# Performance work log

Measured on AMD Instinct MI355X. Metric: run time of the kernel, lower is better.

The kernel has to match this reference:

```python
import jax, jax.numpy as jnp
import numpy as np
import math

B, N, DQ, DK, DV, H = 8, 1024, 512, 512, 512, 8


def setup_inputs() -> dict:
    key = jax.random.key(0)
    ks = jax.random.split(key, 9)
    s = 0.02
    return {
        "Q": jax.random.normal(ks[0], (B, N, DQ), jnp.float32),
        "K": jax.random.normal(ks[1], (B, N, DK), jnp.float32),
        "mask": jax.random.bernoulli(ks[2], 0.9, (B, N)).astype(jnp.float32),
        "Wq": jax.random.normal(ks[3], (DQ, DV), jnp.float32) * s,
        "bq": jnp.zeros((DV,), jnp.float32),
        "Wk": jax.random.normal(ks[4], (DK, DV), jnp.float32) * s,
        "bk": jnp.zeros((DV,), jnp.float32),
        "Wv": jax.random.normal(ks[5], (DK, DV), jnp.float32) * s,
        "bv": jnp.zeros((DV,), jnp.float32),
        "Wo": jax.random.normal(ks[6], (DV, DV), jnp.float32) * s,
        "bo": jnp.zeros((DV,), jnp.float32),
    }


def reference(Q, K, mask, Wq, bq, Wk, bk, Wv, bv, Wo, bo):
    b, n, _ = Q.shape
    dV = Wq.shape[1]
    dh = dV // H
    scale = 1.0 / math.sqrt(dV)
    m = mask[..., None]                      # [B,N,1]
    Qp = (Q @ Wq + bq) * m                   # [B,N,dV]
    Kp = (K @ Wk + bk) * m
    Vp = (K @ Wv + bv) * m
    # torch.cat(x.split(dh,2),0) == head-major stacking -> keep as [H,B,N,dh]
    q = Qp.reshape(b, n, H, dh).transpose(2, 0, 1, 3)
    k = Kp.reshape(b, n, H, dh).transpose(2, 0, 1, 3)
    v = Vp.reshape(b, n, H, dh).transpose(2, 0, 1, 3)
    S = jnp.einsum('hbnd,hbmd->hbnm', q, k) * scale   # [H,B,N,N]
    mx = jnp.max(S, axis=3, keepdims=True)            # unmasked row max (faithful)
    m1 = mask[None, :, :, None]                       # [1,B,N,1]
    m2 = mask[None, :, None, :]                       # [1,B,1,N]
    num = jnp.exp((S - mx) * m1 * m2) * m1 * m2
    A = num / (jnp.sum(num, axis=3, keepdims=True) + 1e-16)
    O = q + jnp.einsum('hbnm,hbmd->hbnd', A, v)       # residual on Q_
    O = O.transpose(1, 2, 0, 3).reshape(b, n, dV)     # un-split heads
    O = O + jax.nn.relu((O @ Wo + bo) * m)
    return O
```

## Files before the change

### kernel.cpp

```cpp
#include <hip/hip_runtime.h>

typedef short bf16x8 __attribute__((ext_vector_type(8)));
typedef float f32x4 __attribute__((ext_vector_type(4)));
typedef float f32x16 __attribute__((ext_vector_type(16)));

#define MFMA16(a, b, c) __builtin_amdgcn_mfma_f32_16x16x32_bf16((a), (b), (c), 0, 0, 0)
#define MFMA32(a, b, c) __builtin_amdgcn_mfma_f32_32x32x16_bf16((a), (b), (c), 0, 0, 0)

#define GLOAD_LDS16(g, l)                                              \
  __builtin_amdgcn_global_load_lds(                                    \
      (const __attribute__((address_space(1))) unsigned int*)(g),      \
      (__attribute__((address_space(3))) unsigned int*)(l), 16, 0, 0)

__device__ __forceinline__ unsigned short f2b(float f) {
  union { float f; unsigned int u; } x; x.f = f;
  unsigned int r = x.u + 0x7FFFu + ((x.u >> 16) & 1u);
  return (unsigned short)(r >> 16);
}
__device__ __forceinline__ float b2f(unsigned short h) {
  union { unsigned int u; float f; } x; x.u = ((unsigned int)h) << 16;
  return x.f;
}
__device__ __forceinline__ unsigned int cvtpk(float lo, float hi) {
  unsigned int r;
  asm("v_cvt_pk_bf16_f32 %0, %1, %2" : "=v"(r) : "v"(lo), "v"(hi));
  return r;
}
__device__ __forceinline__ short cvt1(float x) {
  return (short)(unsigned short)cvtpk(x, x);
}
__device__ __forceinline__ float vexp2(float x) {
  float r;
  asm("v_exp_f32 %0, %1" : "=v"(r) : "v"(x));
  return r;
}

#define SCALE2 0.06375870724f

__global__ __launch_bounds__(256) void wtrans_kernel(
    const float* __restrict__ Wq, const float* __restrict__ Wk,
    const float* __restrict__ Wv, const float* __restrict__ Wo,
    short* __restrict__ Wt) {
  __shared__ float tile[64][65];
  const int z = blockIdx.z;
  const float* W = (z == 0) ? Wq : (z == 1) ? Wk : (z == 2) ? Wv : Wo;
  const float ws = (z == 1) ? SCALE2 : 1.0f;
  const int k0 = blockIdx.x * 64, n0 = blockIdx.y * 64;
  const int t = threadIdx.x;
  const int r = t >> 4, cc = (t & 15) * 4;
#pragma unroll
  for (int it = 0; it < 4; ++it) {
    int row = r + it * 16;
    const float4 v = *(const float4*)(W + (k0 + row) * 512 + n0 + cc);
    tile[row][cc + 0] = v.x; tile[row][cc + 1] = v.y;
    tile[row][cc + 2] = v.z; tile[row][cc + 3] = v.w;
  }
  __syncthreads();
  short* out = Wt + z * (512 * 512);
#pragma unroll
  for (int it = 0; it < 4; ++it) {
    int nrow = r + it * 16;
    unsigned int u0 = cvtpk(tile[cc + 0][nrow] * ws, tile[cc + 1][nrow] * ws);
    unsigned int u1 = cvtpk(tile[cc + 2][nrow] * ws, tile[cc + 3][nrow] * ws);
    uint2 uv; uv.x = u0; uv.y = u1;
    *(uint2*)(out + (n0 + nrow) * 512 + k0 + cc) = uv;
  }
}

__global__ __launch_bounds__(256) void cvt_kernel(
    const float* __restrict__ Q, const float* __restrict__ K,
    const float* __restrict__ mask,
    short* __restrict__ Qb, short* __restrict__ Kb, short* __restrict__ mbf) {
  if (blockIdx.y == 0 && blockIdx.x < 4) {
    int i = (blockIdx.x * 256 + threadIdx.x) * 8;
    float4 a = *(const float4*)(mask + i);
    float4 bb = *(const float4*)(mask + i + 4);
    unsigned int m0 = (a.x != 0.f) ? 0x3F80u : 0u;
    unsigned int m1 = (a.y != 0.f) ? 0x3F80u : 0u;
    unsigned int m2 = (a.z != 0.f) ? 0x3F80u : 0u;
    unsigned int m3 = (a.w != 0.f) ? 0x3F80u : 0u;
    unsigned int m4 = (bb.x != 0.f) ? 0x3F80u : 0u;
    unsigned int m5 = (bb.y != 0.f) ? 0x3F80u : 0u;
    unsigned int m6 = (bb.z != 0.f) ? 0x3F80u : 0u;
    unsigned int m7 = (bb.w != 0.f) ? 0x3F80u : 0u;
    uint4 mm;
    mm.x = m0 | (m1 << 16); mm.y = m2 | (m3 << 16);
    mm.z = m4 | (m5 << 16); mm.w = m6 | (m7 << 16);
    *(uint4*)(mbf + i) = mm;
  }
  const float* src = blockIdx.y ? K : Q;
  short* dst = blockIdx.y ? Kb : Qb;
  int i = (blockIdx.x * 256 + threadIdx.x) * 8;
  float4 v0 = *(const float4*)(src + i);
  float4 v1 = *(const float4*)(src + i + 4);
  uint2 a, b;
  a.x = cvtpk(v0.x, v0.y); a.y = cvtpk(v0.z, v0.w);
  b.x = cvtpk(v1.x, v1.y); b.y = cvtpk(v1.z, v1.w);
  *(uint2*)(dst + i) = a;
  *(uint2*)(dst + i + 4) = b;
}

__device__ __forceinline__ void gemm_bf16_core(
    const short* __restrict__ A, const short* __restrict__ Wt,
    short* Lb, int m0, int t, f32x4 acc[4][4]) {
  const int lane = t & 63, w = t >> 6;
  const int c = lane & 15, g = lane >> 4;
  const int wr = w >> 1, wc = w & 1;
  const int lr = lane >> 3;
  const int sswz = ((lane & 7) ^ lr) << 3;
  const int swc = (c & 7) << 3;
  short* Al = Lb;
  short* Bl = Lb + 8192;

  for (int kt = 0; kt < 8; ++kt) {
#pragma unroll
    for (int it = 0; it < 4; ++it) {
      int row = w * 32 + it * 8;
      GLOAD_LDS16(A + (size_t)(m0 + row + lr) * 512 + kt * 64 + sswz, Al + row * 64);
      GLOAD_LDS16(Wt + (size_t)(row + lr) * 512 + kt * 64 + sswz, Bl + row * 64);
    }
    __syncthreads();
    __builtin_amdgcn_s_setprio(1);
#pragma unroll
    for (int kc = 0; kc < 2; ++kc) {
      bf16x8 af[4], bfr[4];
#pragma unroll
      for (int mi = 0; mi < 4; ++mi) {
        int r = wr * 64 + mi * 16 + c;
        af[mi] = *(const bf16x8*)(Al + r * 64 + ((kc * 32 + 8 * g) ^ swc));
      }
#pragma unroll
      for (int ni = 0; ni < 4; ++ni) {
        int r = wc * 64 + ni * 16 + c;
        bfr[ni] = *(const bf16x8*)(Bl + r * 64 + ((kc * 32 + 8 * g) ^ swc));
      }
#pragma unroll
      for (int mi = 0; mi < 4; ++mi)
#pragma unroll
        for (int ni = 0; ni < 4; ++ni)
          acc[mi][ni] = MFMA16(af[mi], bfr[ni], acc[mi][ni]);
    }
    __builtin_amdgcn_s_setprio(0);
    __syncthreads();
  }
}

__global__ __launch_bounds__(256) void proj2_kernel(
    const short* __restrict__ Qb, const short* __restrict__ Kb,
    const short* __restrict__ Wt4,
    const float* __restrict__ bq, const float* __restrict__ bk, const float* __restrict__ bv,
    const float* __restrict__ maskf,
    short* __restrict__ Qp, short* __restrict__ Kp, short* __restrict__ Vt) {
  __shared__ short Lbuf[16384];
  const int by = blockIdx.y;
  const int m0 = blockIdx.x * 128;
  const int t = threadIdx.x;
  const short* A;
  const short* Wt;
  const float* bias;
  int nbase;
  if (by < 4) { A = Qb; nbase = by * 128; Wt = Wt4 + nbase * 512; bias = bq; }
  else if (by < 8) { A = Kb; nbase = (by - 4) * 128; Wt = Wt4 + 262144 + nbase * 512; bias = bk; }
  else { A = Kb; nbase = (by - 8) * 128; Wt = Wt4 + 524288 + nbase * 512; bias = bv; }
  const float bscale = (by >= 4 && by < 8) ? SCALE2 : 1.0f;

  const f32x4 zz = {0.f, 0.f, 0.f, 0.f};
  f32x4 acc[4][4];
#pragma unroll
  for (int mi = 0; mi < 4; ++mi)
#pragma unroll
    for (int ni = 0; ni < 4; ++ni) acc[mi][ni] = zz;
  gemm_bf16_core(A, Wt, Lbuf, m0, t, acc);

  const int lane = t & 63, w = t >> 6;
  const int c = lane & 15, g = lane >> 4;
  const int wr = w >> 1, wc = w & 1;
  float mk[4][4];
#pragma unroll
  for (int mi = 0; mi < 4; ++mi) {
    int mbase = m0 + wr * 64 + mi * 16 + 4 * g;
#pragma unroll
    for (int i = 0; i < 4; ++i) mk[mi][i] = maskf[mbase + i];
  }
  float bval[4];
#pragma unroll
  for (int ni = 0; ni < 4; ++ni) bval[ni] = bias[nbase + wc * 64 + ni * 16 + c] * bscale;

  if (by < 8) {
#pragma unroll
    for (int ni = 0; ni < 4; ++ni) {
      int nloc = wc * 64 + ni * 16 + c;
#pragma unroll
      for (int mi = 0; mi < 4; ++mi) {
#pragma unroll
        for (int i = 0; i < 4; ++i) {
          int mloc = wr * 64 + mi * 16 + 4 * g + i;
          float v = (acc[mi][ni][i] + bval[ni]) * mk[mi][i];
          Lbuf[mloc * 128 + (nloc ^ ((mloc & 7) << 3))] = cvt1(v);
        }
      }
    }
    __syncthreads();
    short* outp = (by < 4) ? Qp : Kp;
    const int rrow = t >> 4, rcol = (t & 15) * 8;
#pragma unroll
    for (int p = 0; p < 8; ++p) {
      int m = p * 16 + rrow;
      bf16x8 vv = *(const bf16x8*)(Lbuf + m * 128 + (rcol ^ ((m & 7) << 3)));
      *(bf16x8*)(outp + (size_t)(m0 + m) * 512 + nbase + rcol) = vv;
    }
  } else {
#pragma unroll
    for (int ni = 0; ni < 4; ++ni) {
      int nloc = wc * 64 + ni * 16 + c;
#pragma unroll
      for (int mi = 0; mi < 4; ++mi) {
        int mloc4 = wr * 64 + mi * 16 + 4 * g;
        unsigned int lo = cvtpk((acc[mi][ni][0] + bval[ni]) * mk[mi][0],
                                (acc[mi][ni][1] + bval[ni]) * mk[mi][1]);
        unsigned int hi = cvtpk((acc[mi][ni][2] + bval[ni]) * mk[mi][2],
                                (acc[mi][ni][3] + bval[ni]) * mk[mi][3]);
        int ma = (mloc4 & 15) + (((mloc4 >> 4) ^ (nloc & 7)) << 4);
        uint2 uv; uv.x = lo; uv.y = hi;
        *(uint2*)(Lbuf + nloc * 128 + ma) = uv;
      }
    }
    __syncthreads();
    const int rrow = t >> 4, rcol = (t & 15) * 8;
#pragma unroll
    for (int p = 0; p < 8; ++p) {
      int n = p * 16 + rrow;
      int ma = (rcol & 8) + (((rcol >> 4) ^ (n & 7)) << 4);
      bf16x8 vv = *(const bf16x8*)(Lbuf + n * 128 + ma);
      int d = nbase + n;
      int hh = d >> 6, dd = d & 63;
      int mg = m0 + rcol;
      int bi = mg >> 10, seq0 = mg & 1023;
      *(bf16x8*)(Vt + ((size_t)((bi * 8 + hh) * 64 + dd)) * 1024 + seq0) = vv;
    }
  }
}

__global__ __launch_bounds__(128, 3) void attn6_kernel(
    const short* __restrict__ Qp, const short* __restrict__ Kp,
    const short* __restrict__ Vt, const float* __restrict__ mask,
    const short* __restrict__ mbf, short* __restrict__ Obb) {
  __shared__ short Kl[32 * 128];
  __shared__ short Vl[32 * 128];
  __shared__ short Ml[1024];
  const int t = threadIdx.x, lane = t & 63, w = t >> 6;
  const int q32 = lane & 31, hi = lane >> 5;
  const int hw = blockIdx.x;
  const int L = (hw & 7) * 128 + (hw >> 3);
  const int qt = L & 15, head = L >> 4;
  const int b = head & 7, h = head >> 3;
  const int n0 = qt * 64 + w * 32;

  const short* Kg = Kp + (size_t)(b * 1024) * 512 + h * 64;
  const short* Vg = Vt + (size_t)((b * 8 + h) * 64) * 1024;

  bf16x8 qf[4];
  {
    const short* qptr = Qp + ((size_t)(b * 1024 + n0 + q32) * 512 + h * 64 + 8 * hi);
#pragma unroll
    for (int kk = 0; kk < 4; ++kk) qf[kk] = *(const bf16x8*)(qptr + 16 * kk);
  }

  auto STAGE = [&](int kvt) {
    const int kr = kvt * 64;
#pragma unroll
    for (int it = 0; it < 4; ++it) {
      int rb = it * 8 + w * 4;
      int r2 = rb + (lane >> 4);
      int sx = (lane & 15) ^ (r2 & 15);
      GLOAD_LDS16(Kg + (size_t)(kr + 2 * r2 + (sx >> 3)) * 512 + (sx & 7) * 8, Kl + rb * 128);
    }
#pragma unroll
    for (int it = 0; it < 4; ++it) {
      int rb = it * 8 + w * 4;
      int rv = rb + (lane >> 4);
      int sx = (lane & 15) ^ (rv & 15);
      GLOAD_LDS16(Vg + (size_t)(2 * rv + (sx >> 3)) * 1024 + kr + (sx & 7) * 8, Vl + rb * 128);
    }
  };

  GLOAD_LDS16(mbf + b * 1024 + w * 512 + lane * 8, Ml + w * 512);
  STAGE(0);

  f32x16 o0, o1, suma;
#pragma unroll
  for (int e = 0; e < 16; ++e) { o0[e] = 0.f; o1[e] = 0.f; suma[e] = 0.f; }

#pragma unroll 1
  for (int kvt = 0; kvt < 16; ++kvt) {
    asm volatile("s_waitcnt vmcnt(0)" ::: "memory");
    __builtin_amdgcn_sched_barrier(0);
    __builtin_amdgcn_s_barrier();
    __builtin_amdgcn_sched_barrier(0);

#pragma unroll
    for (int half = 0; half < 2; ++half) {
      bf16x8 ka[4], va[2][2], mo[2];
      {
        const int kvr = 32 * half + q32;
        const int r2 = kvr >> 1;
#pragma unroll
        for (int kk = 0; kk < 4; ++kk) {
          int sx = ((((kvr & 1) << 3) | (2 * kk + hi)) ^ (r2 & 15));
          ka[kk] = *(const bf16x8*)(Kl + r2 * 128 + sx * 8);
        }
      }
#pragma unroll
      for (int ds = 0; ds < 2; ++ds) {
        const int d = 32 * ds + q32;
        const int rv = d >> 1;
#pragma unroll
        for (int ch = 0; ch < 2; ++ch) {
          int sx = ((((d & 1) << 3) | (4 * half + 2 * ch + hi)) ^ (rv & 15));
          va[ds][ch] = *(const bf16x8*)(Vl + rv * 128 + sx * 8);
        }
      }
#pragma unroll
      for (int ch = 0; ch < 2; ++ch)
        mo[ch] = *(const bf16x8*)(Ml + kvt * 64 + 32 * half + 16 * ch + 8 * hi);

      __builtin_amdgcn_sched_barrier(0);
      asm volatile("s_waitcnt lgkmcnt(0)" ::: "memory");
      __builtin_amdgcn_sched_barrier(0);
      if (half == 1) {
        __builtin_amdgcn_s_barrier();
        __builtin_amdgcn_sched_barrier(0);
        if (kvt < 15) STAGE(kvt + 1);
        __builtin_amdgcn_sched_barrier(0);
      }

      f32x16 s0;
#pragma unroll
      for (int e = 0; e < 16; ++e) s0[e] = 0.f;
      __builtin_amdgcn_s_setprio(1);
#pragma unroll
      for (int kk = 0; kk < 4; ++kk) s0 = MFMA32(ka[kk], qf[kk], s0);
      __builtin_amdgcn_s_setprio(0);

      f32x16 p0;
#pragma unroll
      for (int e = 0; e < 16; ++e) p0[e] = vexp2(s0[e]);

      bf16x8 pf[2];
#pragma unroll
      for (int ch = 0; ch < 2; ++ch) {
        unsigned int w01a = cvtpk(p0[8 * ch + 0], p0[8 * ch + 1]);
        unsigned int w01b = cvtpk(p0[8 * ch + 2], p0[8 * ch + 3]);
        unsigned int w23a = cvtpk(p0[8 * ch + 4], p0[8 * ch + 5]);
        unsigned int w23b = cvtpk(p0[8 * ch + 6], p0[8 * ch + 7]);
        unsigned int x0 = hi ? w01a : w23a;
        unsigned int x1 = hi ? w01b : w23b;
        unsigned int g0 = (unsigned int)__shfl_xor((int)x0, 32);
        unsigned int g1 = (unsigned int)__shfl_xor((int)x1, 32);
        union { unsigned int u[4]; bf16x8 v; } pu;
        pu.u[0] = hi ? g0 : w01a;
        pu.u[1] = hi ? g1 : w01b;
        pu.u[2] = hi ? w23a : g0;
        pu.u[3] = hi ? w23b : g1;
        pf[ch] = pu.v;
      }

      __builtin_amdgcn_s_setprio(1);
#pragma unroll
      for (int ch = 0; ch < 2; ++ch) {
        o0 = MFMA32(va[0][ch], pf[ch], o0);
        o1 = MFMA32(va[1][ch], pf[ch], o1);
        suma = MFMA32(mo[ch], pf[ch], suma);
      }
      __builtin_amdgcn_s_setprio(0);
    }
  }

  short* Tw = Kl + w * 2304;
  const float inv = __builtin_amdgcn_rcpf(suma[0] + 1e-16f);
#pragma unroll
  for (int rr = 0; rr < 4; ++rr) {
    uint2 uv0, uv1;
    uv0.x = cvtpk(o0[4 * rr + 0] * inv, o0[4 * rr + 1] * inv);
    uv0.y = cvtpk(o0[4 * rr + 2] * inv, o0[4 * rr + 3] * inv);
    *(uint2*)(Tw + q32 * 68 + 8 * rr + 4 * hi) = uv0;
    uv1.x = cvtpk(o1[4 * rr + 0] * inv, o1[4 * rr + 1] * inv);
    uv1.y = cvtpk(o1[4 * rr + 2] * inv, o1[4 * rr + 3] * inv);
    *(uint2*)(Tw + q32 * 68 + 32 + 8 * rr + 4 * hi) = uv1;
  }
  asm volatile("s_waitcnt lgkmcnt(0)" ::: "memory");
  __builtin_amdgcn_sched_barrier(0);

  const int erow = lane >> 1, ecs = (lane & 1) * 8;
  const float mk1 = mask[b * 1024 + n0 + erow];
#pragma unroll
  for (int it = 0; it < 4; ++it) {
    int col = ecs + it * 16;
    bf16x8 av = *(const bf16x8*)(Tw + erow * 68 + col);
    const short* qptr = Qp + (size_t)(b * 1024 + n0 + erow) * 512 + h * 64 + col;
    bf16x8 qv = *(const bf16x8*)qptr;
    uint4 rr;
    rr.x = cvtpk(b2f((unsigned short)qv[0]) + mk1 * b2f((unsigned short)av[0]),
                 b2f((unsigned short)qv[1]) + mk1 * b2f((unsigned short)av[1]));
    rr.y = cvtpk(b2f((unsigned short)qv[2]) + mk1 * b2f((unsigned short)av[2]),
                 b2f((unsigned short)qv[3]) + mk1 * b2f((unsigned short)av[3]));
    rr.z = cvtpk(b2f((unsigned short)qv[4]) + mk1 * b2f((unsigned short)av[4]),
                 b2f((unsigned short)qv[5]) + mk1 * b2f((unsigned short)av[5]));
    rr.w = cvtpk(b2f((unsigned short)qv[6]) + mk1 * b2f((unsigned short)av[6]),
                 b2f((unsigned short)qv[7]) + mk1 * b2f((unsigned short)av[7]));
    *(uint4*)(Obb + (size_t)(b * 1024 + n0 + erow) * 512 + h * 64 + col) = rr;
  }
}

__global__ __launch_bounds__(256) void final2_kernel(
    const short* __restrict__ Obb,
    const short* __restrict__ Wto, const float* __restrict__ bo,
    const float* __restrict__ maskf, float* __restrict__ out) {
  __shared__ short Lbuf[16384];
  const int m0 = blockIdx.x * 128, n0 = blockIdx.y * 128;
  const int t = threadIdx.x;
  const f32x4 zz = {0.f, 0.f, 0.f, 0.f};
  f32x4 acc[4][4];
#pragma unroll
  for (int mi = 0; mi < 4; ++mi)
#pragma unroll
    for (int ni = 0; ni < 4; ++ni) acc[mi][ni] = zz;
  gemm_bf16_core(Obb, Wto + n0 * 512, Lbuf, m0, t, acc);

  const int lane = t & 63, w = t >> 6;
  const int c = lane & 15, g = lane >> 4;
  const int wr = w >> 1, wc = w & 1;
  float mk[4][4];
#pragma unroll
  for (int mi = 0; mi < 4; ++mi) {
    int mbase = m0 + wr * 64 + mi * 16 + 4 * g;
#pragma unroll
    for (int i = 0; i < 4; ++i) mk[mi][i] = maskf[mbase + i];
  }
#pragma unroll
  for (int ni = 0; ni < 4; ++ni) {
    int n = n0 + wc * 64 + ni * 16 + c;
    float bval = bo[n];
#pragma unroll
    for (int mi = 0; mi < 4; ++mi) {
      int mbase = m0 + wr * 64 + mi * 16 + 4 * g;
#pragma unroll
      for (int i = 0; i < 4; ++i) {
        float v = (acc[mi][ni][i] + bval) * mk[mi][i];
        v = fmaxf(v, 0.f);
        size_t off = (size_t)(mbase + i) * 512 + n;
        out[off] = b2f((unsigned short)Obb[off]) + v;
      }
    }
  }
}

extern "C" void kernel_launch(void* const* d_in, const int* in_sizes, int n_in,
                              void* d_out, int out_size, void* d_ws, size_t ws_size,
                              hipStream_t stream) {
  (void)in_sizes; (void)n_in; (void)out_size; (void)ws_size;
  const float* Q    = (const float*)d_in[0];
  const float* K    = (const float*)d_in[1];
  const float* mask = (const float*)d_in[2];
  const float* Wq   = (const float*)d_in[3];
  const float* bq   = (const float*)d_in[4];
  const float* Wk   = (const float*)d_in[5];
  const float* bk   = (const float*)d_in[6];
  const float* Wv   = (const float*)d_in[7];
  const float* bv   = (const float*)d_in[8];
  const float* Wo   = (const float*)d_in[9];
  const float* bo   = (const float*)d_in[10];

  char* ws = (char*)d_ws;
  const size_t MB = 1048576;
  short* Wt4 = (short*)ws;
  short* Qb  = (short*)(ws + 2 * MB);
  short* Kb  = (short*)(ws + 10 * MB);
  short* Qp  = (short*)(ws + 18 * MB);
  short* Kp  = (short*)(ws + 26 * MB);
  short* Vt  = (short*)(ws + 34 * MB);
  short* Obb = (short*)(ws + 42 * MB);
  short* mbf = (short*)(ws + 50 * MB);
  float* out = (float*)d_out;

  wtrans_kernel<<<dim3(8, 8, 4), 256, 0, stream>>>(Wq, Wk, Wv, Wo, Wt4);
  cvt_kernel<<<dim3(2048, 2), 256, 0, stream>>>(Q, K, mask, Qb, Kb, mbf);
  proj2_kernel<<<dim3(64, 12), 256, 0, stream>>>(Qb, Kb, Wt4, bq, bk, bv, mask, Qp, Kp, Vt);
  attn6_kernel<<<dim3(1024), 128, 0, stream>>>(Qp, Kp, Vt, mask, mbf, Obb);
  final2_kernel<<<dim3(64, 4), 256, 0, stream>>>(Obb, Wt4 + 3 * 262144, bo, mask, out);
}
```

Baseline: 82.79 us.

## Double-buffer K/V tiles in attention and merge prep kernels into one launch

The attention kernel now keeps two LDS buffers for K and V and prefetches two tiles ahead, waiting on a partial vmcnt so global loads overlap compute more deeply. The weight-transpose and input-conversion kernels are merged into a single launch to remove one launch. Doubling the K/V shared memory raises LDS use per block, which may limit occupancy.

```diff
diff --git a/kernel.cpp b/kernel.cpp
--- a/kernel.cpp
+++ b/kernel.cpp
@@ -37,67 +37,72 @@
 
 #define SCALE2 0.06375870724f
 
-__global__ __launch_bounds__(256) void wtrans_kernel(
+__global__ __launch_bounds__(256) void prep_kernel(
     const float* __restrict__ Wq, const float* __restrict__ Wk,
     const float* __restrict__ Wv, const float* __restrict__ Wo,
-    short* __restrict__ Wt) {
-  __shared__ float tile[64][65];
-  const int z = blockIdx.z;
-  const float* W = (z == 0) ? Wq : (z == 1) ? Wk : (z == 2) ? Wv : Wo;
-  const float ws = (z == 1) ? SCALE2 : 1.0f;
-  const int k0 = blockIdx.x * 64, n0 = blockIdx.y * 64;
-  const int t = threadIdx.x;
-  const int r = t >> 4, cc = (t & 15) * 4;
-#pragma unroll
-  for (int it = 0; it < 4; ++it) {
-    int row = r + it * 16;
-    const float4 v = *(const float4*)(W + (k0 + row) * 512 + n0 + cc);
-    tile[row][cc + 0] = v.x; tile[row][cc + 1] = v.y;
-    tile[row][cc + 2] = v.z; tile[row][cc + 3] = v.w;
-  }
-  __syncthreads();
-  short* out = Wt + z * (512 * 512);
-#pragma unroll
-  for (int it = 0; it < 4; ++it) {
-    int nrow = r + it * 16;
-    unsigned int u0 = cvtpk(tile[cc + 0][nrow] * ws, tile[cc + 1][nrow] * ws);
-    unsigned int u1 = cvtpk(tile[cc + 2][nrow] * ws, tile[cc + 3][nrow] * ws);
-    uint2 uv; uv.x = u0; uv.y = u1;
-    *(uint2*)(out + (n0 + nrow) * 512 + k0 + cc) = uv;
-  }
-}
-
-__global__ __launch_bounds__(256) void cvt_kernel(
     const float* __restrict__ Q, const float* __restrict__ K,
     const float* __restrict__ mask,
-    short* __restrict__ Qb, short* __restrict__ Kb, short* __restrict__ mbf) {
-  if (blockIdx.y == 0 && blockIdx.x < 4) {
-    int i = (blockIdx.x * 256 + threadIdx.x) * 8;
-    float4 a = *(const float4*)(mask + i);
-    float4 bb = *(const float4*)(mask + i + 4);
-    unsigned int m0 = (a.x != 0.f) ? 0x3F80u : 0u;
-    unsigned int m1 = (a.y != 0.f) ? 0x3F80u : 0u;
-    unsigned int m2 = (a.z != 0.f) ? 0x3F80u : 0u;
-    unsigned int m3 = (a.w != 0.f) ? 0x3F80u : 0u;
-    unsigned int m4 = (bb.x != 0.f) ? 0x3F80u : 0u;
-    unsigned int m5 = (bb.y != 0.f) ? 0x3F80u : 0u;
-    unsigned int m6 = (bb.z != 0.f) ? 0x3F80u : 0u;
-    unsigned int m7 = (bb.w != 0.f) ? 0x3F80u : 0u;
-    uint4 mm;
-    mm.x = m0 | (m1 << 16); mm.y = m2 | (m3 << 16);
-    mm.z = m4 | (m5 << 16); mm.w = m6 | (m7 << 16);
-    *(uint4*)(mbf + i) = mm;
-  }
-  const float* src = blockIdx.y ? K : Q;
-  short* dst = blockIdx.y ? Kb : Qb;
-  int i = (blockIdx.x * 256 + threadIdx.x) * 8;
-  float4 v0 = *(const float4*)(src + i);
-  float4 v1 = *(const float4*)(src + i + 4);
-  uint2 a, b;
-  a.x = cvtpk(v0.x, v0.y); a.y = cvtpk(v0.z, v0.w);
-  b.x = cvtpk(v1.x, v1.y); b.y = cvtpk(v1.z, v1.w);
-  *(uint2*)(dst + i) = a;
-  *(uint2*)(dst + i + 4) = b;
+    short* __restrict__ Wt, short* __restrict__ Qb, short* __restrict__ Kb,
+    short* __restrict__ mbf) {
+  __shared__ float tile[64][65];
+  const int bid = blockIdx.x;
+  const int t = threadIdx.x;
+  if (bid < 256) {
+    const int z = bid >> 6;
+    const int rem = bid & 63;
+    const int k0 = (rem >> 3) * 64, n0 = (rem & 7) * 64;
+    const float* W = (z == 0) ? Wq : (z == 1) ? Wk : (z == 2) ? Wv : Wo;
+    const float ws = (z == 1) ? SCALE2 : 1.0f;
+    const int r = t >> 4, cc = (t & 15) * 4;
+#pragma unroll
+    for (int it = 0; it < 4; ++it) {
+      int row = r + it * 16;
+      const float4 v = *(const float4*)(W + (k0 + row) * 512 + n0 + cc);
+      tile[row][cc + 0] = v.x; tile[row][cc + 1] = v.y;
+      tile[row][cc + 2] = v.z; tile[row][cc + 3] = v.w;
+    }
+    __syncthreads();
+    short* out = Wt + z * (512 * 512);
+#pragma unroll
+    for (int it = 0; it < 4; ++it) {
+      int nrow = r + it * 16;
+      unsigned int u0 = cvtpk(tile[cc + 0][nrow] * ws, tile[cc + 1][nrow] * ws);
+      unsigned int u1 = cvtpk(tile[cc + 2][nrow] * ws, tile[cc + 3][nrow] * ws);
+      uint2 uv; uv.x = u0; uv.y = u1;
+      *(uint2*)(out + (n0 + nrow) * 512 + k0 + cc) = uv;
+    }
+  } else {
+    const int idx = bid - 256;
+    const int ybit = idx >> 11;
+    const int x = idx & 2047;
+    if (ybit == 0 && x < 4) {
+      int i = (x * 256 + t) * 8;
+      float4 a = *(const float4*)(mask + i);
+      float4 bb = *(const float4*)(mask + i + 4);
+      unsigned int m0 = (a.x != 0.f) ? 0x3F80u : 0u;
+      unsigned int m1 = (a.y != 0.f) ? 0x3F80u : 0u;
+      unsigned int m2 = (a.z != 0.f) ? 0x3F80u : 0u;
+      unsigned int m3 = (a.w != 0.f) ? 0x3F80u : 0u;
+      unsigned int m4 = (bb.x != 0.f) ? 0x3F80u : 0u;
+      unsigned int m5 = (bb.y != 0.f) ? 0x3F80u : 0u;
+      unsigned int m6 = (bb.z != 0.f) ? 0x3F80u : 0u;
+      unsigned int m7 = (bb.w != 0.f) ? 0x3F80u : 0u;
+      uint4 mm;
+      mm.x = m0 | (m1 << 16); mm.y = m2 | (m3 << 16);
+      mm.z = m4 | (m5 << 16); mm.w = m6 | (m7 << 16);
+      *(uint4*)(mbf + i) = mm;
+    }
+    const float* src = ybit ? K : Q;
+    short* dst = ybit ? Kb : Qb;
+    int i = (x * 256 + t) * 8;
+    float4 v0 = *(const float4*)(src + i);
+    float4 v1 = *(const float4*)(src + i + 4);
+    uint2 a, b;
+    a.x = cvtpk(v0.x, v0.y); a.y = cvtpk(v0.z, v0.w);
+    b.x = cvtpk(v1.x, v1.y); b.y = cvtpk(v1.z, v1.w);
+    *(uint2*)(dst + i) = a;
+    *(uint2*)(dst + i + 4) = b;
+  }
 }
 
 __device__ __forceinline__ void gemm_bf16_core(
@@ -241,12 +246,12 @@
   }
 }
 
-__global__ __launch_bounds__(128, 3) void attn6_kernel(
+__global__ __launch_bounds__(128, 3) void attn7_kernel(
     const short* __restrict__ Qp, const short* __restrict__ Kp,
     const short* __restrict__ Vt, const float* __restrict__ mask,
     const short* __restrict__ mbf, short* __restrict__ Obb) {
-  __shared__ short Kl[32 * 128];
-  __shared__ short Vl[32 * 128];
+  __shared__ short Kl[2][32 * 128];
+  __shared__ short Vl[2][32 * 128];
   __shared__ short Ml[1024];
   const int t = threadIdx.x, lane = t & 63, w = t >> 6;
   const int q32 = lane & 31, hi = lane >> 5;
@@ -265,27 +270,32 @@
 #pragma unroll
     for (int kk = 0; kk < 4; ++kk) qf[kk] = *(const bf16x8*)(qptr + 16 * kk);
   }
-
-  auto STAGE = [&](int kvt) {
+  asm volatile("s_waitcnt vmcnt(0)" ::: "memory");
+  __builtin_amdgcn_sched_barrier(0);
+
+  auto STAGE = [&](int kvt, int buf) {
     const int kr = kvt * 64;
+    short* Kd = &Kl[buf][0];
+    short* Vd = &Vl[buf][0];
 #pragma unroll
     for (int it = 0; it < 4; ++it) {
       int rb = it * 8 + w * 4;
       int r2 = rb + (lane >> 4);
       int sx = (lane & 15) ^ (r2 & 15);
-      GLOAD_LDS16(Kg + (size_t)(kr + 2 * r2 + (sx >> 3)) * 512 + (sx & 7) * 8, Kl + rb * 128);
+      GLOAD_LDS16(Kg + (size_t)(kr + 2 * r2 + (sx >> 3)) * 512 + (sx & 7) * 8, Kd + rb * 128);
     }
 #pragma unroll
     for (int it = 0; it < 4; ++it) {
       int rb = it * 8 + w * 4;
       int rv = rb + (lane >> 4);
       int sx = (lane & 15) ^ (rv & 15);
-      GLOAD_LDS16(Vg + (size_t)(2 * rv + (sx >> 3)) * 1024 + kr + (sx & 7) * 8, Vl + rb * 128);
+      GLOAD_LDS16(Vg + (size_t)(2 * rv + (sx >> 3)) * 1024 + kr + (sx & 7) * 8, Vd + rb * 128);
     }
   };
 
   GLOAD_LDS16(mbf + b * 1024 + w * 512 + lane * 8, Ml + w * 512);
-  STAGE(0);
+  STAGE(0, 0);
+  STAGE(1, 1);
 
   f32x16 o0, o1, suma;
 #pragma unroll
@@ -293,7 +303,9 @@
 
 #pragma unroll 1
   for (int kvt = 0; kvt < 16; ++kvt) {
-    asm volatile("s_waitcnt vmcnt(0)" ::: "memory");
+    const int cur = kvt & 1;
+    if (kvt < 15) { asm volatile("s_waitcnt vmcnt(8)" ::: "memory"); }
+    else          { asm volatile("s_waitcnt vmcnt(0)" ::: "memory"); }
     __builtin_amdgcn_sched_barrier(0);
     __builtin_amdgcn_s_barrier();
     __builtin_amdgcn_sched_barrier(0);
@@ -307,7 +319,7 @@
 #pragma unroll
         for (int kk = 0; kk < 4; ++kk) {
           int sx = ((((kvr & 1) << 3) | (2 * kk + hi)) ^ (r2 & 15));
-          ka[kk] = *(const bf16x8*)(Kl + r2 * 128 + sx * 8);
+          ka[kk] = *(const bf16x8*)(&Kl[cur][0] + r2 * 128 + sx * 8);
         }
       }
 #pragma unroll
@@ -317,7 +329,7 @@
 #pragma unroll
         for (int ch = 0; ch < 2; ++ch) {
           int sx = ((((d & 1) << 3) | (4 * half + 2 * ch + hi)) ^ (rv & 15));
-          va[ds][ch] = *(const bf16x8*)(Vl + rv * 128 + sx * 8);
+          va[ds][ch] = *(const bf16x8*)(&Vl[cur][0] + rv * 128 + sx * 8);
         }
       }
 #pragma unroll
@@ -330,7 +342,7 @@
       if (half == 1) {
         __builtin_amdgcn_s_barrier();
         __builtin_amdgcn_sched_barrier(0);
-        if (kvt < 15) STAGE(kvt + 1);
+        if (kvt < 14) STAGE(kvt + 2, cur);
         __builtin_amdgcn_sched_barrier(0);
       }
 
@@ -376,7 +388,7 @@
     }
   }
 
-  short* Tw = Kl + w * 2304;
+  short* Tw = &Kl[0][0] + w * 2304;
   const float inv = __builtin_amdgcn_rcpf(suma[0] + 1e-16f);
 #pragma unroll
   for (int rr = 0; rr < 4; ++rr) {
@@ -483,9 +495,8 @@
   short* mbf = (short*)(ws + 50 * MB);
   float* out = (float*)d_out;
 
-  wtrans_kernel<<<dim3(8, 8, 4), 256, 0, stream>>>(Wq, Wk, Wv, Wo, Wt4);
-  cvt_kernel<<<dim3(2048, 2), 256, 0, stream>>>(Q, K, mask, Qb, Kb, mbf);
+  prep_kernel<<<dim3(4352), 256, 0, stream>>>(Wq, Wk, Wv, Wo, Q, K, mask, Wt4, Qb, Kb, mbf);
   proj2_kernel<<<dim3(64, 12), 256, 0, stream>>>(Qb, Kb, Wt4, bq, bk, bv, mask, Qp, Kp, Vt);
-  attn6_kernel<<<dim3(1024), 128, 0, stream>>>(Qp, Kp, Vt, mask, mbf, Obb);
+  attn7_kernel<<<dim3(1024), 128, 0, stream>>>(Qp, Kp, Vt, mask, mbf, Obb);
   final2_kernel<<<dim3(64, 4), 256, 0, stream>>>(Obb, Wt4 + 3 * 262144, bo, mask, out);
 }
```

Measured after the change: 79.75 us (median of 3 runs). 1.04x faster.
